# Optimization experiments

Hardware: AMD Instinct MI355X
Metric: run time of the kernel (lower is better)

Reference implementation:

```python
import jax, jax.numpy as jnp
import numpy as np

N_EMBD = 1024
N_HEAD = 16
B, T = 2, 2048


def setup_inputs() -> dict:
    key = jax.random.key(0)
    k1, k2, k3 = jax.random.split(key, 3)
    scale = 1.0 / np.sqrt(N_EMBD)
    x = jax.random.normal(k1, (B, T, N_EMBD), dtype=jnp.float32)
    W_qkv = jax.random.normal(k2, (N_EMBD, 3 * N_EMBD), dtype=jnp.float32) * scale
    b_qkv = jnp.zeros((3 * N_EMBD,), dtype=jnp.float32)
    W_proj = jax.random.normal(k3, (N_EMBD, N_EMBD), dtype=jnp.float32) * scale
    b_proj = jnp.zeros((N_EMBD,), dtype=jnp.float32)
    return {"x": x, "W_qkv": W_qkv, "b_qkv": b_qkv, "W_proj": W_proj, "b_proj": b_proj}


def reference(x, W_qkv, b_qkv, W_proj, b_proj):
    Bx, Tx, C = x.shape
    H = N_HEAD
    D = C // H  # head_size
    qkv = x @ W_qkv + b_qkv  # [B,T,3C]
    Q, K, V = jnp.split(qkv, 3, axis=2)
    # [B,T,C] -> [B,H,T,D]
    Q = Q.reshape(Bx, Tx, H, D).transpose(0, 2, 1, 3)
    K = K.reshape(Bx, Tx, H, D).transpose(0, 2, 1, 3)
    V = V.reshape(Bx, Tx, H, D).transpose(0, 2, 1, 3)
    scores = jnp.einsum("bhqd,bhkd->bhqk", Q, K) / jnp.sqrt(jnp.float32(D))
    causal = jnp.tril(jnp.ones((Tx, Tx), dtype=bool))
    scores = jnp.where(causal, scores, jnp.float32(-jnp.inf))
    weights = jax.nn.softmax(scores, axis=-1)
    out = jnp.einsum("bhqk,bhkd->bhqd", weights, V)  # [B,H,T,D]
    out = out.transpose(0, 2, 1, 3).reshape(Bx, Tx, C)
    return out @ W_proj + b_proj
```

## Files before the change

kernel.cpp:

```cpp
#include <hip/hip_runtime.h>
#include <hip/hip_bf16.h>
#include <math.h>

#define BB 2
#define TT 2048
#define CC 1024
#define HH 16
#define DD 64
#define C3 3072
#define BT 4096

typedef __attribute__((ext_vector_type(8))) short short8;
typedef __attribute__((ext_vector_type(8))) unsigned short ushort8;
typedef __attribute__((ext_vector_type(4))) unsigned short ushort4v;
typedef __attribute__((ext_vector_type(4))) float floatx4;

__device__ __forceinline__ unsigned short f2b(float f) {
    union { float f; unsigned int u; } v; v.f = f;
    unsigned int u = v.u;
    unsigned int r = (u + 0x7fffu + ((u >> 16) & 1u)) >> 16;
    return (unsigned short)r;
}
__device__ __forceinline__ unsigned short f2b_fast(float f) {
    unsigned int u = __builtin_bit_cast(unsigned int, f);
    return (unsigned short)((u + 0x8000u) >> 16);
}

__device__ __forceinline__ void store_out(unsigned short* p, float v) { *p = f2b(v); }
__device__ __forceinline__ void store_out(float* p, float v) { *p = v; }

__device__ __forceinline__ void async16(const unsigned short* g, unsigned short* lds) {
    __builtin_amdgcn_global_load_lds(
        (const __attribute__((address_space(1))) unsigned int*)g,
        (__attribute__((address_space(3))) unsigned int*)lds, 16, 0, 0);
}

__global__ __launch_bounds__(256) void prep_kernel(
    const float* __restrict__ x, unsigned short* __restrict__ xb,
    const float* __restrict__ Wqkv, const float* __restrict__ Wproj,
    unsigned short* __restrict__ Wqkv_t, unsigned short* __restrict__ Wproj_t)
{
    __shared__ float tile[64 * 65];
    const int tid = threadIdx.x;
    const int bid = blockIdx.x;

    if (bid < 2048) {
        int i = bid * 256 + tid;
        const float4 v0 = *(const float4*)&x[(size_t)i * 8];
        const float4 v1 = *(const float4*)&x[(size_t)i * 8 + 4];
        ushort8 pk;
        pk[0] = f2b(v0.x); pk[1] = f2b(v0.y); pk[2] = f2b(v0.z); pk[3] = f2b(v0.w);
        pk[4] = f2b(v1.x); pk[5] = f2b(v1.y); pk[6] = f2b(v1.z); pk[7] = f2b(v1.w);
        *(ushort8*)&xb[(size_t)i * 8] = pk;
        return;
    }

    const int xt = bid - 2048;
    const int cxt = xt & 63;
    const int r0  = (xt >> 6) * 64;
    const float* src; unsigned short* dst; int Ccols, c0;
    if (cxt < 48) { src = Wqkv;  dst = Wqkv_t;  Ccols = C3; c0 = cxt * 64; }
    else          { src = Wproj; dst = Wproj_t; Ccols = CC; c0 = (cxt - 48) * 64; }
#pragma unroll
    for (int it = 0; it < 4; it++) {
        int idx = it * 256 + tid;
        int row = idx >> 4;
        int c4  = idx & 15;
        float4 v = *(const float4*)&src[(size_t)(r0 + row) * Ccols + c0 + c4 * 4];
        tile[row * 65 + c4 * 4 + 0] = v.x;
        tile[row * 65 + c4 * 4 + 1] = v.y;
        tile[row * 65 + c4 * 4 + 2] = v.z;
        tile[row * 65 + c4 * 4 + 3] = v.w;
    }
    __syncthreads();
#pragma unroll
    for (int it = 0; it < 2; it++) {
        int idx = it * 256 + tid;
        int orow = idx >> 3;
        int o8   = idx & 7;
        ushort8 pk;
#pragma unroll
        for (int j = 0; j < 8; j++) pk[j] = f2b(tile[(o8 * 8 + j) * 65 + orow]);
        *(ushort8*)&dst[(size_t)(c0 + orow) * CC + r0 + o8 * 8] = pk;
    }
}

template <typename OUT_T, bool WVT>
__global__ __launch_bounds__(256) void gemm_bt_kernel(
    const unsigned short* __restrict__ A, const unsigned short* __restrict__ Bm,
    const float* __restrict__ bias, OUT_T* __restrict__ Cmat,
    unsigned short* __restrict__ Vt,
    int M, int N, int K, float qscale, int qcols)
{
    __shared__ __align__(16) unsigned short sA[128 * 64];
    __shared__ __align__(16) unsigned short sB[128 * 64];

    const int tid = threadIdx.x;
    const int lane16 = tid & 15, quad = (tid & 63) >> 4;
    const int w = tid >> 6;
    const int wm = w >> 1, wn = w & 1;
    const int m0 = blockIdx.y * 128, n0 = blockIdx.x * 128;
    const int lx = lane16 & 7;

    floatx4 acc[4][4] = {};

    for (int kt = 0; kt < K; kt += 64) {
#pragma unroll
        for (int it = 0; it < 4; it++) {
            int idx = it * 256 + tid;
            int row = idx >> 3;
            int c8m = (idx & 7) ^ (row & 7);
            int wslot = it * 256 + (tid & 192);
            async16(&A[(size_t)(m0 + row) * K + kt + c8m * 8], &sA[wslot * 8]);
            async16(&Bm[(size_t)(n0 + row) * K + kt + c8m * 8], &sB[wslot * 8]);
        }
        __syncthreads();
#pragma unroll
        for (int ks = 0; ks < 64; ks += 32) {
            const int slot = ((ks >> 3) + quad) ^ lx;
            short8 af[4], bf[4];
#pragma unroll
            for (int t = 0; t < 4; t++) {
                af[t] = *(const short8*)&sA[(wm * 64 + t * 16 + lane16) * 64 + slot * 8];
                bf[t] = *(const short8*)&sB[(wn * 64 + t * 16 + lane16) * 64 + slot * 8];
            }
#pragma unroll
            for (int mt = 0; mt < 4; mt++)
#pragma unroll
                for (int nt = 0; nt < 4; nt++)
                    acc[mt][nt] = __builtin_amdgcn_mfma_f32_16x16x32_bf16(
                        af[mt], bf[nt], acc[mt][nt], 0, 0, 0);
        }
        __syncthreads();
    }

#pragma unroll
    for (int mt = 0; mt < 4; mt++) {
#pragma unroll
        for (int nt = 0; nt < 4; nt++) {
            int col = n0 + wn * 64 + nt * 16 + lane16;
            float bv = bias[col];
            float sc = (col < qcols) ? qscale : 1.0f;
            float v[4];
            int row0 = m0 + wm * 64 + mt * 16 + quad * 4;
#pragma unroll
            for (int r = 0; r < 4; r++) {
                v[r] = (acc[mt][nt][r] + bv) * sc;
                store_out(&Cmat[(size_t)(row0 + r) * N + col], v[r]);
            }
            if (WVT && n0 >= 2 * CC) {
                int hd = col - 2 * CC;
                int b  = row0 >> 11;
                int token = row0 & (TT - 1);
                ushort4v pk;
#pragma unroll
                for (int r = 0; r < 4; r++) pk[r] = f2b(v[r]);
                *(ushort4v*)&Vt[((size_t)(b * HH * DD) + hd) * TT + token] = pk;
            }
        }
    }
}

__global__ __launch_bounds__(256) void attn_mfma_kernel(
    const unsigned short* __restrict__ qkv, const unsigned short* __restrict__ Vt,
    unsigned short* __restrict__ att)
{
    __shared__ __align__(16) unsigned short Ks[64 * 72];
    __shared__ __align__(16) unsigned short Vs[64 * 72];
    __shared__ __align__(16) unsigned short Pl[64 * 76];

    const int tid = threadIdx.x;
    const int l = tid & 63;
    const int lane16 = l & 15, quad = l >> 4;
    const int w = tid >> 6;
    const int bh = blockIdx.x;
    const int b = bh >> 4, h = bh & 15;
    const int g = blockIdx.y;

    const int srow = tid >> 3;
    const int sc8  = (tid & 7) * 8;
    const unsigned short* kbase = &qkv[(size_t)(b * TT) * C3 + CC + h * DD + sc8];
    const unsigned short* vbase = &Vt[(size_t)(bh * DD + srow) * TT + sc8];

#pragma unroll
    for (int pass = 0; pass < 2; ++pass) {
        const int p  = pass ? g : (31 - g);
        const int q0 = p * 64;
        const int qw = q0 + w * 16;

        short8 qf[2];
        {
            const unsigned short* qp =
                &qkv[(size_t)(b * TT + qw + lane16) * C3 + h * DD + quad * 8];
            qf[0] = *(const short8*)&qp[0];
            qf[1] = *(const short8*)&qp[32];
        }

        float psum[4] = {0.f, 0.f, 0.f, 0.f};
        floatx4 O[4] = {};

        ushort8 kr0 = *(const ushort8*)&kbase[(size_t)srow * C3];
        ushort8 kr1 = *(const ushort8*)&kbase[(size_t)(srow + 32) * C3];
        ushort8 vr0 = *(const ushort8*)&vbase[0];
        ushort8 vr1 = *(const ushort8*)&vbase[(size_t)32 * TT];

        const int ntiles = p + 1;
        for (int t = 0; t < ntiles; ++t) {
            const int k0 = t * 64;
            __syncthreads();
            *(ushort8*)&Ks[srow * 72 + sc8]        = kr0;
            *(ushort8*)&Ks[(srow + 32) * 72 + sc8] = kr1;
            *(ushort8*)&Vs[srow * 72 + sc8]        = vr0;
            *(ushort8*)&Vs[(srow + 32) * 72 + sc8] = vr1;
            __syncthreads();

            if (t + 1 < ntiles) {
                const int kn = k0 + 64;
                kr0 = *(const ushort8*)&kbase[(size_t)(kn + srow) * C3];
                kr1 = *(const ushort8*)&kbase[(size_t)(kn + srow + 32) * C3];
                vr0 = *(const ushort8*)&vbase[kn];
                vr1 = *(const ushort8*)&vbase[(size_t)32 * TT + kn];
            }

            floatx4 s4[4] = {};
#pragma unroll
            for (int nt = 0; nt < 4; nt++) {
                short8 kf0 = *(const short8*)&Ks[(nt * 16 + lane16) * 72 + quad * 8];
                short8 kf1 = *(const short8*)&Ks[(nt * 16 + lane16) * 72 + 32 + quad * 8];
                s4[nt] = __builtin_amdgcn_mfma_f32_16x16x32_bf16(qf[0], kf0, s4[nt], 0, 0, 0);
                s4[nt] = __builtin_amdgcn_mfma_f32_16x16x32_bf16(qf[1], kf1, s4[nt], 0, 0, 0);
            }

            const bool diag = (t == ntiles - 1);
#pragma unroll
            for (int nt = 0; nt < 4; nt++) {
                int key = k0 + nt * 16 + lane16;
#pragma unroll
                for (int r = 0; r < 4; r++) {
                    float v = s4[nt][r];
                    if (diag) v = (key > qw + quad * 4 + r) ? -1e30f : v;
                    float pe = exp2f(v);
                    psum[r] += pe;
                    Pl[(w * 16 + quad * 4 + r) * 76 + nt * 16 + lane16] = f2b_fast(pe);
                }
            }
            __threadfence_block();

            short8 pf0 = *(const short8*)&Pl[(w * 16 + lane16) * 76 + quad * 8];
            short8 pf1 = *(const short8*)&Pl[(w * 16 + lane16) * 76 + 32 + quad * 8];
#pragma unroll
            for (int dt = 0; dt < 4; dt++) {
                short8 vf0 = *(const short8*)&Vs[(dt * 16 + lane16) * 72 + quad * 8];
                short8 vf1 = *(const short8*)&Vs[(dt * 16 + lane16) * 72 + 32 + quad * 8];
                O[dt] = __builtin_amdgcn_mfma_f32_16x16x32_bf16(pf0, vf0, O[dt], 0, 0, 0);
                O[dt] = __builtin_amdgcn_mfma_f32_16x16x32_bf16(pf1, vf1, O[dt], 0, 0, 0);
            }
        }

#pragma unroll
        for (int off = 1; off <= 8; off <<= 1)
#pragma unroll
            for (int r = 0; r < 4; r++)
                psum[r] += __shfl_xor(psum[r], off, 64);

        float rl[4];
#pragma unroll
        for (int r = 0; r < 4; r++) rl[r] = 1.0f / psum[r];
#pragma unroll
        for (int dt = 0; dt < 4; dt++)
#pragma unroll
            for (int r = 0; r < 4; r++) {
                int qq = qw + quad * 4 + r;
                int d = dt * 16 + lane16;
                att[(size_t)(b * TT + qq) * CC + h * DD + d] = f2b(O[dt][r] * rl[r]);
            }
    }
}

extern "C" void kernel_launch(void* const* d_in, const int* in_sizes, int n_in,
                              void* d_out, int out_size, void* d_ws, size_t ws_size,
                              hipStream_t stream) {
    const float* x     = (const float*)d_in[0];
    const float* Wqkv  = (const float*)d_in[1];
    const float* bqkv  = (const float*)d_in[2];
    const float* Wproj = (const float*)d_in[3];
    const float* bproj = (const float*)d_in[4];
    float* out = (float*)d_out;

    unsigned short* xb      = (unsigned short*)d_ws;
    unsigned short* qkv_b   = xb      + (size_t)BT * CC;
    unsigned short* Wqkv_t  = qkv_b   + (size_t)BT * C3;
    unsigned short* Wproj_t = Wqkv_t  + (size_t)C3 * CC;
    unsigned short* Vt      = Wproj_t + (size_t)CC * CC;
    unsigned short* att_b   = Vt      + (size_t)BB * HH * DD * TT;

    prep_kernel<<<3072, 256, 0, stream>>>(x, xb, Wqkv, Wproj, Wqkv_t, Wproj_t);

    {
        dim3 grid(C3 / 128, BT / 128);
        gemm_bt_kernel<unsigned short, true><<<grid, 256, 0, stream>>>(
            xb, Wqkv_t, bqkv, qkv_b, Vt, BT, C3, CC, 0.125f * 1.44269504f, CC);
    }
    {
        dim3 grid(BB * HH, 16);
        attn_mfma_kernel<<<grid, 256, 0, stream>>>(qkv_b, Vt, att_b);
    }
    {
        dim3 grid(CC / 128, BT / 128);
        gemm_bt_kernel<float, false><<<grid, 256, 0, stream>>>(
            att_b, Wproj_t, bproj, out, nullptr, BT, CC, CC, 1.0f, 0);
    }
}
```

Baseline: 185.9 us.

## Use 32x32 MFMA with 128-key tiles and split keys across waves

The attention kernel now loads 128-key K/V tiles per iteration and arranges its four waves as 2 query groups × 2 key halves. Each wave computes a 32×64 score tile with mfma_f32_32x32x16_bf16 instead of 16×16 MFMAs. The two key-half partial outputs and row sums are combined at the end through shared memory, which reuses the K/V buffers. The aim is fewer barriers per key and larger MFMAs with better operand reuse, at the cost of more registers, a final cross-wave reduction, and idle waves on diagonal tiles when the key count is odd.

```diff
diff --git a/kernel.cpp b/kernel.cpp
--- a/kernel.cpp
+++ b/kernel.cpp
@@ -14,6 +14,7 @@
 typedef __attribute__((ext_vector_type(8))) unsigned short ushort8;
 typedef __attribute__((ext_vector_type(4))) unsigned short ushort4v;
 typedef __attribute__((ext_vector_type(4))) float floatx4;
+typedef __attribute__((ext_vector_type(16))) float floatx16;
 
 __device__ __forceinline__ unsigned short f2b(float f) {
     union { float f; unsigned int u; } v; v.f = f;
@@ -165,115 +166,147 @@
     const unsigned short* __restrict__ qkv, const unsigned short* __restrict__ Vt,
     unsigned short* __restrict__ att)
 {
-    __shared__ __align__(16) unsigned short Ks[64 * 72];
-    __shared__ __align__(16) unsigned short Vs[64 * 72];
-    __shared__ __align__(16) unsigned short Pl[64 * 76];
+    __shared__ __align__(16) unsigned short Ks[128 * 72];
+    __shared__ __align__(16) unsigned short Vs[64 * 136];
+    __shared__ __align__(16) unsigned short Pl[64 * 132];
 
     const int tid = threadIdx.x;
-    const int l = tid & 63;
-    const int lane16 = l & 15, quad = l >> 4;
+    const int lane = tid & 63;
+    const int ln31 = lane & 31, half = lane >> 5;
     const int w = tid >> 6;
-    const int bh = blockIdx.x;
+    const int wq = w & 1, wk = w >> 1;
+    const int g  = blockIdx.x;
+    const int bh = blockIdx.y;
     const int b = bh >> 4, h = bh & 15;
-    const int g = blockIdx.y;
-
-    const int srow = tid >> 3;
-    const int sc8  = (tid & 7) * 8;
-    const unsigned short* kbase = &qkv[(size_t)(b * TT) * C3 + CC + h * DD + sc8];
-    const unsigned short* vbase = &Vt[(size_t)(bh * DD + srow) * TT + sc8];
-
-#pragma unroll
+
+    const int kcol = (tid & 7) * 8,  krow0 = tid >> 3;
+    const int vcol = (tid & 15) * 8, vrow0 = tid >> 4;
+
+    const unsigned short* kgbase = &qkv[(size_t)(b * TT) * C3 + CC + h * DD + kcol];
+    const unsigned short* vgbase = &Vt[(size_t)(bh * DD) * TT + vcol];
+
+    float* Oswf = (float*)Ks;
+    float* psw  = (float*)Vs;
+
     for (int pass = 0; pass < 2; ++pass) {
         const int p  = pass ? g : (31 - g);
-        const int q0 = p * 64;
-        const int qw = q0 + w * 16;
-
-        short8 qf[2];
+        const int qb = p * 64 + wq * 32;
+
+        short8 qf[4];
         {
             const unsigned short* qp =
-                &qkv[(size_t)(b * TT + qw + lane16) * C3 + h * DD + quad * 8];
-            qf[0] = *(const short8*)&qp[0];
-            qf[1] = *(const short8*)&qp[32];
-        }
-
-        float psum[4] = {0.f, 0.f, 0.f, 0.f};
-        floatx4 O[4] = {};
-
-        ushort8 kr0 = *(const ushort8*)&kbase[(size_t)srow * C3];
-        ushort8 kr1 = *(const ushort8*)&kbase[(size_t)(srow + 32) * C3];
-        ushort8 vr0 = *(const ushort8*)&vbase[0];
-        ushort8 vr1 = *(const ushort8*)&vbase[(size_t)32 * TT];
-
-        const int ntiles = p + 1;
-        for (int t = 0; t < ntiles; ++t) {
-            const int k0 = t * 64;
+                &qkv[(size_t)(b * TT + qb + ln31) * C3 + h * DD + half * 8];
+#pragma unroll
+            for (int s = 0; s < 4; s++) qf[s] = *(const short8*)&qp[s * 16];
+        }
+
+        float psum[16] = {};
+        floatx16 O[2] = {};
+
+        const int J = (p >> 1) + 1;
+
+        ushort8 kpre[4], vpre[4];
+#pragma unroll
+        for (int it = 0; it < 4; it++) {
+            kpre[it] = *(const ushort8*)&kgbase[(size_t)(krow0 + 32 * it) * C3];
+            vpre[it] = *(const ushort8*)&vgbase[(size_t)(vrow0 + 16 * it) * TT];
+        }
+
+        for (int j = 0; j < J; ++j) {
+            const int kb = j * 128;
             __syncthreads();
-            *(ushort8*)&Ks[srow * 72 + sc8]        = kr0;
-            *(ushort8*)&Ks[(srow + 32) * 72 + sc8] = kr1;
-            *(ushort8*)&Vs[srow * 72 + sc8]        = vr0;
-            *(ushort8*)&Vs[(srow + 32) * 72 + sc8] = vr1;
+#pragma unroll
+            for (int it = 0; it < 4; it++) {
+                *(ushort8*)&Ks[(krow0 + 32 * it) * 72 + kcol] = kpre[it];
+                *(ushort8*)&Vs[(vrow0 + 16 * it) * 136 + vcol] = vpre[it];
+            }
             __syncthreads();
 
-            if (t + 1 < ntiles) {
-                const int kn = k0 + 64;
-                kr0 = *(const ushort8*)&kbase[(size_t)(kn + srow) * C3];
-                kr1 = *(const ushort8*)&kbase[(size_t)(kn + srow + 32) * C3];
-                vr0 = *(const ushort8*)&vbase[kn];
-                vr1 = *(const ushort8*)&vbase[(size_t)32 * TT + kn];
-            }
-
-            floatx4 s4[4] = {};
-#pragma unroll
-            for (int nt = 0; nt < 4; nt++) {
-                short8 kf0 = *(const short8*)&Ks[(nt * 16 + lane16) * 72 + quad * 8];
-                short8 kf1 = *(const short8*)&Ks[(nt * 16 + lane16) * 72 + 32 + quad * 8];
-                s4[nt] = __builtin_amdgcn_mfma_f32_16x16x32_bf16(qf[0], kf0, s4[nt], 0, 0, 0);
-                s4[nt] = __builtin_amdgcn_mfma_f32_16x16x32_bf16(qf[1], kf1, s4[nt], 0, 0, 0);
-            }
-
-            const bool diag = (t == ntiles - 1);
-#pragma unroll
-            for (int nt = 0; nt < 4; nt++) {
-                int key = k0 + nt * 16 + lane16;
-#pragma unroll
-                for (int r = 0; r < 4; r++) {
-                    float v = s4[nt][r];
-                    if (diag) v = (key > qw + quad * 4 + r) ? -1e30f : v;
-                    float pe = exp2f(v);
-                    psum[r] += pe;
-                    Pl[(w * 16 + quad * 4 + r) * 76 + nt * 16 + lane16] = f2b_fast(pe);
+            if (j + 1 < J) {
+                const int kn = kb + 128;
+#pragma unroll
+                for (int it = 0; it < 4; it++) {
+                    kpre[it] = *(const ushort8*)&kgbase[(size_t)(kn + krow0 + 32 * it) * C3];
+                    vpre[it] = *(const ushort8*)&vgbase[(size_t)(vrow0 + 16 * it) * TT + kn];
                 }
             }
-            __threadfence_block();
-
-            short8 pf0 = *(const short8*)&Pl[(w * 16 + lane16) * 76 + quad * 8];
-            short8 pf1 = *(const short8*)&Pl[(w * 16 + lane16) * 76 + 32 + quad * 8];
-#pragma unroll
-            for (int dt = 0; dt < 4; dt++) {
-                short8 vf0 = *(const short8*)&Vs[(dt * 16 + lane16) * 72 + quad * 8];
-                short8 vf1 = *(const short8*)&Vs[(dt * 16 + lane16) * 72 + 32 + quad * 8];
-                O[dt] = __builtin_amdgcn_mfma_f32_16x16x32_bf16(pf0, vf0, O[dt], 0, 0, 0);
-                O[dt] = __builtin_amdgcn_mfma_f32_16x16x32_bf16(pf1, vf1, O[dt], 0, 0, 0);
-            }
-        }
-
-#pragma unroll
-        for (int off = 1; off <= 8; off <<= 1)
-#pragma unroll
-            for (int r = 0; r < 4; r++)
-                psum[r] += __shfl_xor(psum[r], off, 64);
-
-        float rl[4];
-#pragma unroll
-        for (int r = 0; r < 4; r++) rl[r] = 1.0f / psum[r];
-#pragma unroll
-        for (int dt = 0; dt < 4; dt++)
-#pragma unroll
-            for (int r = 0; r < 4; r++) {
-                int qq = qw + quad * 4 + r;
-                int d = dt * 16 + lane16;
-                att[(size_t)(b * TT + qq) * CC + h * DD + d] = f2b(O[dt][r] * rl[r]);
-            }
+
+            const int tk = 2 * j + wk;
+            if (tk <= p) {
+                const int klocal = wk * 64;
+
+                floatx16 s4[2] = {};
+#pragma unroll
+                for (int nt = 0; nt < 2; nt++) {
+                    const int krow = klocal + nt * 32 + ln31;
+#pragma unroll
+                    for (int s = 0; s < 4; s++) {
+                        short8 kf = *(const short8*)&Ks[krow * 72 + s * 16 + half * 8];
+                        s4[nt] = __builtin_amdgcn_mfma_f32_32x32x16_bf16(qf[s], kf, s4[nt], 0, 0, 0);
+                    }
+                }
+
+                const bool diag = (tk == p);
+#pragma unroll
+                for (int nt = 0; nt < 2; nt++) {
+                    const int key = kb + klocal + nt * 32 + ln31;
+#pragma unroll
+                    for (int reg = 0; reg < 16; reg++) {
+                        const int qrow = (reg & 3) + 8 * (reg >> 2) + 4 * half;
+                        float v = s4[nt][reg];
+                        if (diag) v = (key > qb + qrow) ? -1e30f : v;
+                        float pe = exp2f(v);
+                        psum[reg] += pe;
+                        Pl[(wq * 32 + qrow) * 132 + klocal + nt * 32 + ln31] = f2b_fast(pe);
+                    }
+                }
+                __threadfence_block();
+
+                short8 pf[4];
+#pragma unroll
+                for (int ks = 0; ks < 4; ks++)
+                    pf[ks] = *(const short8*)&Pl[(wq * 32 + ln31) * 132 + klocal + ks * 16 + half * 8];
+#pragma unroll
+                for (int dt = 0; dt < 2; dt++) {
+                    const int vrow = dt * 32 + ln31;
+#pragma unroll
+                    for (int ks = 0; ks < 4; ks++) {
+                        short8 vf = *(const short8*)&Vs[vrow * 136 + klocal + ks * 16 + half * 8];
+                        O[dt] = __builtin_amdgcn_mfma_f32_32x32x16_bf16(pf[ks], vf, O[dt], 0, 0, 0);
+                    }
+                }
+            }
+        }
+
+#pragma unroll
+        for (int off = 1; off <= 16; off <<= 1)
+#pragma unroll
+            for (int reg = 0; reg < 16; reg++)
+                psum[reg] += __shfl_xor(psum[reg], off, 64);
+
+        __syncthreads();
+        if (wk == 1) {
+#pragma unroll
+            for (int reg = 0; reg < 16; reg++) {
+                const int qrow = (reg & 3) + 8 * (reg >> 2) + 4 * half;
+                Oswf[(wq * 32 + qrow) * 64 + ln31]      = O[0][reg];
+                Oswf[(wq * 32 + qrow) * 64 + 32 + ln31] = O[1][reg];
+                psw[wq * 32 + qrow] = psum[reg];
+            }
+        }
+        __syncthreads();
+        if (wk == 0) {
+#pragma unroll
+            for (int reg = 0; reg < 16; reg++) {
+                const int qrow = (reg & 3) + 8 * (reg >> 2) + 4 * half;
+                const float rl = 1.0f / (psum[reg] + psw[wq * 32 + qrow]);
+                const size_t obase = (size_t)(b * TT + qb + qrow) * CC + h * DD;
+                float v0 = O[0][reg] + Oswf[(wq * 32 + qrow) * 64 + ln31];
+                float v1 = O[1][reg] + Oswf[(wq * 32 + qrow) * 64 + 32 + ln31];
+                att[obase + ln31]      = f2b(v0 * rl);
+                att[obase + 32 + ln31] = f2b(v1 * rl);
+            }
+        }
     }
 }
 
@@ -302,7 +335,7 @@
             xb, Wqkv_t, bqkv, qkv_b, Vt, BT, C3, CC, 0.125f * 1.44269504f, CC);
     }
     {
-        dim3 grid(BB * HH, 16);
+        dim3 grid(16, BB * HH);
         attn_mfma_kernel<<<grid, 256, 0, stream>>>(qkv_b, Vt, att_b);
     }
     {
```

Result: slower. 222.8 us (+19.9%).
